# Kernel optimization log

Hardware: AMD Instinct MI355X
Metric: run time of the kernel (lower is better)

The kernel has to match this reference:

```python
import jax, jax.numpy as jnp
import numpy as np

B, T, H = 1, 2048, 2048
HEADS, DH = 16, 128  # head_dim = H // HEADS
K = 50               # block size
NEG = -1e9


def setup_inputs() -> dict:
    key = jax.random.key(0)
    ks = jax.random.split(key, 6)
    x = jax.random.normal(ks[0], (B, T, H), jnp.float32)
    mask = jnp.ones((B, T), jnp.float32)
    bias = jax.random.normal(ks[1], (B, HEADS, T, T), jnp.float32) * 0.02
    s = 1.0 / np.sqrt(H)
    Wq = jax.random.normal(ks[2], (H, HEADS, DH), jnp.float32) * s
    Wk = jax.random.normal(ks[3], (H, HEADS, DH), jnp.float32) * s
    Wv = jax.random.normal(ks[4], (H, HEADS, DH), jnp.float32) * s
    Wo = jax.random.normal(ks[5], (HEADS, DH, H), jnp.float32) * (1.0 / np.sqrt(H))
    return {"x_BxTxH": x, "mask_BxT": mask, "attention_bias_BxHxTxT": bias,
            "Wq": Wq, "Wk": Wk, "Wv": Wv, "Wo": Wo}


def _local_self_attention(x, mask, bias, Wq, Wk, Wv, Wo):
    b, t, h = x.shape
    extra = K - t % K          # module always pads (pads a full block if t % K == 0)
    p = t + extra
    n = p // K
    # pad + block the inputs: [b, n, K, h]
    xb = jnp.pad(x, ((0, 0), (0, extra), (0, 0))).reshape(b, n, K, h)
    # pad mask with -1e9 (as in the module), block, build pairwise mask via multiply
    mb = jnp.pad(mask, ((0, 0), (0, extra)), constant_values=NEG).reshape(b, n, K)
    pair = mb[..., :, None] * mb[..., None, :]              # [b, n, K, K]
    mask_bias = jnp.where(pair > 0, 0.0, NEG)[:, :, None]   # [b, n, 1, K, K] (broadcast heads)
    # pad attention bias and extract block-diagonal: [b, n, heads, K, K]
    bp = jnp.pad(bias, ((0, 0), (0, 0), (0, extra), (0, extra)))
    nb = bp.reshape(b, HEADS, n, K, n, K)
    idx = jnp.arange(n)
    blk_bias = nb[:, :, idx, :, idx, :]          # [n, b, heads, K, K]
    blk_bias = jnp.transpose(blk_bias, (1, 0, 2, 3, 4))  # [b, n, heads, K, K]
    # per-block multi-head attention (no qkv bias, query scaled by head_dim**-0.5)
    q = jnp.einsum('bnkh,hef->bnkef', xb, Wq) * (DH ** -0.5)
    k = jnp.einsum('bnkh,hef->bnkef', xb, Wk)
    v = jnp.einsum('bnkh,hef->bnkef', xb, Wv)
    logits = jnp.einsum('bnqef,bnkef->bneqk', q, k) + blk_bias + mask_bias
    attn = jax.nn.softmax(logits, axis=-1)
    out = jnp.einsum('bneqk,bnkef->bnqef', attn, v)
    out = jnp.einsum('bnqef,efh->bnqh', out, Wo).reshape(b, p, h)
    return out[:, :t, :]


def reference(x_BxTxH, mask_BxT, attention_bias_BxHxTxT, Wq, Wk, Wv, Wo):
    return _local_self_attention(x_BxTxH, mask_BxT, attention_bias_BxHxTxT, Wq, Wk, Wv, Wo)
```

## Files before the change

kernel.cpp:

```cpp
#include <hip/hip_runtime.h>
#include <hip/hip_bf16.h>

typedef _Float16 f16x8 __attribute__((ext_vector_type(8)));
typedef float f32x4 __attribute__((ext_vector_type(4)));

#define T_DIM 2048
#define H_DIM 2048
#define N_HEADS 16
#define DH 128
#define KBLK 50
#define NBLK 41
#define NEGV (-1.0e9f)
#define QSCALE 0.08838834764831845f

__device__ __forceinline__ void gl_lds16(const void* g, void* l) {
    __builtin_amdgcn_global_load_lds(
        (const __attribute__((address_space(1))) void*)g,
        (__attribute__((address_space(3))) void*)l, 16, 0, 0);
}

__global__ __launch_bounds__(256) void prep_kernel(const float* __restrict__ x,
                                                   const float* __restrict__ Wq,
                                                   const float* __restrict__ Wk,
                                                   const float* __restrict__ Wv,
                                                   const float* __restrict__ Wo,
                                                   _Float16* __restrict__ xb,
                                                   _Float16* __restrict__ WT,
                                                   _Float16* __restrict__ WoT) {
    __shared__ float tile[32][33];
    int z = blockIdx.z;
    int tx = threadIdx.x, ty = threadIdx.y;
    if (z == 4) {
        if (blockIdx.y >= 32) return;
        int flat = blockIdx.y * 64 + blockIdx.x;
        int i = (flat * 256 + ty * 32 + tx) * 8;
        float4 a = *(const float4*)&x[i];
        float4 b = *(const float4*)&x[i + 4];
        f16x8 o = {(_Float16)a.x, (_Float16)a.y, (_Float16)a.z, (_Float16)a.w,
                   (_Float16)b.x, (_Float16)b.y, (_Float16)b.z, (_Float16)b.w};
        *(f16x8*)&xb[i] = o;
        return;
    }
    const float* src = (z == 0) ? Wq : (z == 1) ? Wk : (z == 2) ? Wv : Wo;
    _Float16* dst = (z == 3) ? WoT : (WT + (size_t)z * T_DIM * H_DIM);
    int bx = blockIdx.x * 32, by = blockIdx.y * 32;
#pragma unroll
    for (int i = 0; i < 4; i++)
        tile[ty + i * 8][tx] = src[(size_t)(by + ty + i * 8) * H_DIM + bx + tx];
    __syncthreads();
#pragma unroll
    for (int i = 0; i < 4; i++)
        dst[(size_t)(bx + ty + i * 8) * H_DIM + by + tx] = (_Float16)tile[tx][ty + i * 8];
}

__global__ __launch_bounds__(512, 2) void qkv192_kernel(const _Float16* __restrict__ A,
                                                        const _Float16* __restrict__ BT,
                                                        _Float16* __restrict__ qkv) {
    const int K = 2048, NT = 32;
    __shared__ _Float16 smem[57344];
    _Float16* sA0 = smem;
    _Float16* sA1 = smem + 16384;
    _Float16* sB0 = smem + 32768;
    _Float16* sB1 = smem + 45056;

    int tid = threadIdx.x;
    int lane = tid & 63, wave = tid >> 6;
    int wm = wave >> 2, wn = wave & 3;
    int cb = lane & 15, hi = lane >> 4;

    int bid = blockIdx.x;
    int swz = (bid & 7) * 32 + (bid >> 3);
    int by = swz >> 5, bx = swz & 31;
    int bm = by * 256, bn = bx * 192;

    f32x4 acc[8][3];
#pragma unroll
    for (int m = 0; m < 8; m++)
#pragma unroll
        for (int n = 0; n < 3; n++) acc[m][n] = (f32x4){0.f, 0.f, 0.f, 0.f};

    int rp = tid >> 3, cc = tid & 7;
    int scol = ((cc ^ (rp & 7)) << 3);

    auto stageA = [&](int t, int u) {
        int buf = t & 1;
        gl_lds16(A + (size_t)(bm + u * 64 + rp) * K + (t << 6) + scol,
                 (buf ? sA1 : sA0) + u * 4096 + tid * 8);
    };
    auto stageB = [&](int t, int u) {
        int buf = t & 1;
        gl_lds16(BT + (size_t)(bn + u * 64 + rp) * K + (t << 6) + scol,
                 (buf ? sB1 : sB0) + u * 4096 + tid * 8);
    };

    f16x8 a_lo[4][2], a_hi[4][2], b01[2][2], b2[2];

    stageA(0, 0); stageA(0, 1); stageA(0, 2); stageA(0, 3);
    stageB(0, 0); stageB(0, 1); stageB(0, 2);
    stageA(1, 0); stageA(1, 1); stageA(1, 2); stageA(1, 3);
    asm volatile("s_waitcnt vmcnt(4)" ::: "memory");
    __builtin_amdgcn_s_barrier();

    for (int t = 0; t < NT; t++) {
        int buf = t & 1;
        const char* bA = (const char*)(buf ? sA1 : sA0);
        const char* bB = (const char*)(buf ? sB1 : sB0);
#pragma unroll
        for (int mf = 0; mf < 4; mf++) {
            int ra = wm * 128 + mf * 16 + cb;
#pragma unroll
            for (int ks = 0; ks < 2; ks++)
                a_lo[mf][ks] = *(const f16x8*)(bA + (ra << 7) +
                                               ((ks * 64 + hi * 16) ^ ((ra & 7) << 4)));
        }
#pragma unroll
        for (int nf = 0; nf < 2; nf++) {
            int rb = wn * 48 + nf * 16 + cb;
#pragma unroll
            for (int ks = 0; ks < 2; ks++)
                b01[nf][ks] = *(const f16x8*)(bB + (rb << 7) +
                                              ((ks * 64 + hi * 16) ^ ((rb & 7) << 4)));
        }
        if (t + 1 < NT) { stageB(t + 1, 0); stageB(t + 1, 1); }
        __builtin_amdgcn_s_barrier();
        asm volatile("s_waitcnt lgkmcnt(0)" ::: "memory");
        __builtin_amdgcn_s_setprio(1);
#pragma unroll
        for (int mf = 0; mf < 4; mf++)
#pragma unroll
            for (int nf = 0; nf < 2; nf++)
#pragma unroll
                for (int ks = 0; ks < 2; ks++)
                    acc[mf][nf] = __builtin_amdgcn_mfma_f32_16x16x32_f16(a_lo[mf][ks], b01[nf][ks], acc[mf][nf], 0, 0, 0);
        __builtin_amdgcn_s_setprio(0);
        __builtin_amdgcn_s_barrier();

#pragma unroll
        for (int mf = 0; mf < 4; mf++) {
            int ra = wm * 128 + 64 + mf * 16 + cb;
#pragma unroll
            for (int ks = 0; ks < 2; ks++)
                a_hi[mf][ks] = *(const f16x8*)(bA + (ra << 7) +
                                               ((ks * 64 + hi * 16) ^ ((ra & 7) << 4)));
        }
        {
            int rb = wn * 48 + 32 + cb;
#pragma unroll
            for (int ks = 0; ks < 2; ks++)
                b2[ks] = *(const f16x8*)(bB + (rb << 7) +
                                         ((ks * 64 + hi * 16) ^ ((rb & 7) << 4)));
        }
        if (t + 1 < NT) stageB(t + 1, 2);
        __builtin_amdgcn_s_barrier();
        asm volatile("s_waitcnt lgkmcnt(0)" ::: "memory");
        __builtin_amdgcn_s_setprio(1);
#pragma unroll
        for (int mf = 0; mf < 4; mf++)
#pragma unroll
            for (int ks = 0; ks < 2; ks++)
                acc[4 + mf][2] = __builtin_amdgcn_mfma_f32_16x16x32_f16(a_hi[mf][ks], b2[ks], acc[4 + mf][2], 0, 0, 0);
        __builtin_amdgcn_s_setprio(0);
        __builtin_amdgcn_s_barrier();

        if (t + 2 < NT) { stageA(t + 2, 0); stageA(t + 2, 1); }
        __builtin_amdgcn_s_barrier();
        __builtin_amdgcn_s_setprio(1);
#pragma unroll
        for (int mf = 0; mf < 4; mf++)
#pragma unroll
            for (int ks = 0; ks < 2; ks++)
                acc[mf][2] = __builtin_amdgcn_mfma_f32_16x16x32_f16(a_lo[mf][ks], b2[ks], acc[mf][2], 0, 0, 0);
        __builtin_amdgcn_s_setprio(0);
        __builtin_amdgcn_s_barrier();

        if (t + 2 < NT) { stageA(t + 2, 2); stageA(t + 2, 3); }
        if (t < NT - 2)
            asm volatile("s_waitcnt vmcnt(4)" ::: "memory");
        else if (t == NT - 2)
            asm volatile("s_waitcnt vmcnt(0)" ::: "memory");
        __builtin_amdgcn_s_barrier();
        __builtin_amdgcn_s_setprio(1);
#pragma unroll
        for (int mf = 0; mf < 4; mf++)
#pragma unroll
            for (int nf = 0; nf < 2; nf++)
#pragma unroll
                for (int ks = 0; ks < 2; ks++)
                    acc[4 + mf][nf] = __builtin_amdgcn_mfma_f32_16x16x32_f16(a_hi[mf][ks], b01[nf][ks], acc[4 + mf][nf], 0, 0, 0);
        __builtin_amdgcn_s_setprio(0);
        __builtin_amdgcn_s_barrier();
    }

#pragma unroll
    for (int p = 0; p < 2; p++) {
        if (p) __builtin_amdgcn_s_barrier();
        if (wm == p) {
#pragma unroll
            for (int mf = 0; mf < 8; mf++)
#pragma unroll
                for (int nf = 0; nf < 3; nf++) {
                    int col = wn * 48 + nf * 16 + cb;
                    float sc = ((bn + col) >> 11) == 0 ? QSCALE : 1.0f;
#pragma unroll
                    for (int r = 0; r < 4; r++) {
                        int row = mf * 16 + hi * 4 + r;
                        smem[row * 200 + col] = (_Float16)(acc[mf][nf][r] * sc);
                    }
                }
        }
        __builtin_amdgcn_s_barrier();
#pragma unroll
        for (int it = 0; it < 6; it++) {
            int c = it * 512 + tid;
            int row = c / 24, col8 = c - row * 24;
            int gm = bm + p * 128 + row;
            int gn = bn + col8 * 8;
            int tensor = gn >> 11;
            int ef = gn & 2047;
            int e = ef >> 7, f0 = ef & 127;
            uint4 v = *(const uint4*)&smem[row * 200 + col8 * 8];
            *(uint4*)(qkv + (size_t)tensor * (T_DIM * H_DIM) + (size_t)e * (T_DIM * DH) +
                      (size_t)gm * DH + f0) = v;
        }
    }
}

__global__ __launch_bounds__(512, 2) void oproj_kernel(const _Float16* __restrict__ A,
                                                       const _Float16* __restrict__ BT,
                                                       _Float16* __restrict__ part) {
    const int K = 2048, NT = 8;
    __shared__ _Float16 smem[65536];
    _Float16* sA0 = smem;
    _Float16* sA1 = smem + 16384;
    _Float16* sB0 = smem + 32768;
    _Float16* sB1 = smem + 49152;

    int tid = threadIdx.x;
    int lane = tid & 63, wave = tid >> 6;
    int wm = wave >> 2, wn = wave & 3;
    int cb = lane & 15, hi = lane >> 4;

    int bid = blockIdx.x;
    int s = bid & 3, tile = bid >> 2;
    int by = tile >> 3, bx = tile & 7;
    int bm = by * 256, bn = bx * 256;
    int kbase = s * 512;

    f32x4 acc[8][4];
#pragma unroll
    for (int m = 0; m < 8; m++)
#pragma unroll
        for (int n = 0; n < 4; n++) acc[m][n] = (f32x4){0.f, 0.f, 0.f, 0.f};

    auto stageP = [&](int t, int p) {
        int buf = t & 1, k0 = kbase + (t << 6);
        const _Float16* src = (p < 2) ? A + (size_t)(bm + ((p & 1) << 7)) * K + k0
                                      : BT + (size_t)(bn + ((p & 1) << 7)) * K + k0;
        _Float16* dst = ((p < 2) ? (buf ? sA1 : sA0) : (buf ? sB1 : sB0)) + ((p & 1) << 13);
#pragma unroll
        for (int l = 0; l < 2; l++) {
            int c = l * 512 + tid;
            int rp = c >> 3, cc = c & 7;
            int col = (cc ^ (rp & 7)) << 3;
            gl_lds16(src + (size_t)rp * K + col, dst + c * 8);
        }
    };

    f16x8 a_lo[4][2], a_hi[4][2], b_lo[2][2], b_hi[2][2];

    stageP(0, 0); stageP(0, 1); stageP(0, 2); stageP(0, 3);
    stageP(1, 0); stageP(1, 1);
    asm volatile("s_waitcnt vmcnt(4)" ::: "memory");
    __builtin_amdgcn_s_barrier();

    for (int t = 0; t < NT; t++) {
        int buf = t & 1;
        const char* bA = (const char*)(buf ? sA1 : sA0);
        const char* bB = (const char*)(buf ? sB1 : sB0);
#pragma unroll
        for (int m = 0; m < 4; m++) {
            int ra = wm * 128 + m * 16 + cb;
#pragma unroll
            for (int ks = 0; ks < 2; ks++)
                a_lo[m][ks] = *(const f16x8*)(bA + (ra << 7) +
                                              ((ks * 64 + hi * 16) ^ ((ra & 7) << 4)));
        }
#pragma unroll
        for (int n = 0; n < 2; n++) {
            int rb = wn * 64 + n * 16 + cb;
#pragma unroll
            for (int ks = 0; ks < 2; ks++)
                b_lo[n][ks] = *(const f16x8*)(bB + (rb << 7) +
                                              ((ks * 64 + hi * 16) ^ ((rb & 7) << 4)));
        }
        if (t + 1 < NT) stageP(t + 1, 2);
        __builtin_amdgcn_s_barrier();
        asm volatile("s_waitcnt lgkmcnt(0)" ::: "memory");
        __builtin_amdgcn_s_setprio(1);
#pragma unroll
        for (int m = 0; m < 4; m++)
#pragma unroll
            for (int n = 0; n < 2; n++)
#pragma unroll
                for (int ks = 0; ks < 2; ks++)
                    acc[m][n] = __builtin_amdgcn_mfma_f32_16x16x32_f16(a_lo[m][ks], b_lo[n][ks], acc[m][n], 0, 0, 0);
        __builtin_amdgcn_s_setprio(0);
        __builtin_amdgcn_s_barrier();

#pragma unroll
        for (int m = 0; m < 4; m++) {
            int ra = wm * 128 + 64 + m * 16 + cb;
#pragma unroll
            for (int ks = 0; ks < 2; ks++)
                a_hi[m][ks] = *(const f16x8*)(bA + (ra << 7) +
                                              ((ks * 64 + hi * 16) ^ ((ra & 7) << 4)));
        }
#pragma unroll
        for (int n = 0; n < 2; n++) {
            int rb = wn * 64 + 32 + n * 16 + cb;
#pragma unroll
            for (int ks = 0; ks < 2; ks++)
                b_hi[n][ks] = *(const f16x8*)(bB + (rb << 7) +
                                              ((ks * 64 + hi * 16) ^ ((rb & 7) << 4)));
        }
        if (t + 1 < NT) stageP(t + 1, 3);
        __builtin_amdgcn_s_barrier();
        asm volatile("s_waitcnt lgkmcnt(0)" ::: "memory");
        __builtin_amdgcn_s_setprio(1);
#pragma unroll
        for (int m = 0; m < 4; m++)
#pragma unroll
            for (int n = 0; n < 2; n++)
#pragma unroll
                for (int ks = 0; ks < 2; ks++)
                    acc[4 + m][2 + n] = __builtin_amdgcn_mfma_f32_16x16x32_f16(a_hi[m][ks], b_hi[n][ks], acc[4 + m][2 + n], 0, 0, 0);
        __builtin_amdgcn_s_setprio(0);
        __builtin_amdgcn_s_barrier();

        if (t + 2 < NT) stageP(t + 2, 0);
        __builtin_amdgcn_s_barrier();
        __builtin_amdgcn_s_setprio(1);
#pragma unroll
        for (int m = 0; m < 4; m++)
#pragma unroll
            for (int n = 0; n < 2; n++)
#pragma unroll
                for (int ks = 0; ks < 2; ks++)
                    acc[m][2 + n] = __builtin_amdgcn_mfma_f32_16x16x32_f16(a_lo[m][ks], b_hi[n][ks], acc[m][2 + n], 0, 0, 0);
        __builtin_amdgcn_s_setprio(0);
        __builtin_amdgcn_s_barrier();

        if (t + 2 < NT) stageP(t + 2, 1);
        if (t < NT - 2)
            asm volatile("s_waitcnt vmcnt(4)" ::: "memory");
        else if (t == NT - 2)
            asm volatile("s_waitcnt vmcnt(0)" ::: "memory");
        __builtin_amdgcn_s_barrier();
        __builtin_amdgcn_s_setprio(1);
#pragma unroll
        for (int m = 0; m < 4; m++)
#pragma unroll
            for (int n = 0; n < 2; n++)
#pragma unroll
                for (int ks = 0; ks < 2; ks++)
                    acc[4 + m][n] = __builtin_amdgcn_mfma_f32_16x16x32_f16(a_hi[m][ks], b_lo[n][ks], acc[4 + m][n], 0, 0, 0);
        __builtin_amdgcn_s_setprio(0);
        __builtin_amdgcn_s_barrier();
    }

    _Float16* pb = part + (size_t)s * T_DIM * H_DIM;
#pragma unroll
    for (int p = 0; p < 2; p++) {
        if (p) __builtin_amdgcn_s_barrier();
        if (wm == p) {
#pragma unroll
            for (int m = 0; m < 8; m++)
#pragma unroll
                for (int n = 0; n < 4; n++) {
                    int col = wn * 64 + ((n & 1) * 16) + ((n >> 1) * 32) + cb;
#pragma unroll
                    for (int r = 0; r < 4; r++) {
                        int row = ((m & 3) * 16) + ((m >> 2) * 64) + hi * 4 + r;
                        smem[row * 264 + col] = (_Float16)acc[m][n][r];
                    }
                }
        }
        __builtin_amdgcn_s_barrier();
#pragma unroll
        for (int it = 0; it < 8; it++) {
            int c = it * 512 + tid;
            int row = c >> 5, col8 = c & 31;
            int gm = bm + p * 128 + row;
            int gn = bn + col8 * 8;
            uint4 v = *(const uint4*)&smem[row * 264 + col8 * 8];
            *(uint4*)&pb[(size_t)gm * H_DIM + gn] = v;
        }
    }
}

__global__ __launch_bounds__(256) void reduce4_kernel(const _Float16* __restrict__ part,
                                                      float* __restrict__ out) {
    const size_t S = (size_t)T_DIM * H_DIM;
    int i = (blockIdx.x * 256 + threadIdx.x) * 8;
    f16x8 p0 = *(const f16x8*)&part[i];
    f16x8 p1 = *(const f16x8*)&part[S + i];
    f16x8 p2 = *(const f16x8*)&part[2 * S + i];
    f16x8 p3 = *(const f16x8*)&part[3 * S + i];
#pragma unroll
    for (int j = 0; j < 8; j++)
        out[i + j] = (float)p0[j] + (float)p1[j] + (float)p2[j] + (float)p3[j];
}

__global__ __launch_bounds__(256) void attn_kernel(const _Float16* __restrict__ qkvb,
                                                   const float* __restrict__ bias,
                                                   const float* __restrict__ mask,
                                                   _Float16* __restrict__ aout) {
    int bid = blockIdx.x;
    int n = bid >> 4, e = bid & 15;
    int t0 = n * KBLK;
    int valid = (T_DIM - t0 < KBLK) ? (T_DIM - t0) : KBLK;

    __shared__ _Float16 Qs[64 * 136];
    __shared__ _Float16 Ks[64 * 136];
    __shared__ _Float16 VTs[128 * 72];
    __shared__ _Float16 Ps[64 * 72];
    __shared__ float maskv[64];

    int tid = threadIdx.x;
    int lane = tid & 63, wave = tid >> 6;
    const _Float16* qp = qkvb + (size_t)e * (T_DIM * DH);
    const _Float16* kp = qkvb + (size_t)(T_DIM * H_DIM) + (size_t)e * (T_DIM * DH);
    const _Float16* vp = qkvb + (size_t)2 * (T_DIM * H_DIM) + (size_t)e * (T_DIM * DH);

#pragma unroll
    for (int i = 0; i < 4; i++) {
        int c = tid + i * 256;
        int r = c >> 4, c8 = c & 15;
        uint4 z = {0u, 0u, 0u, 0u};
        uint4 vq = z, vk = z;
        if (r < valid) {
            vq = *(const uint4*)&qp[(size_t)(t0 + r) * DH + c8 * 8];
            vk = *(const uint4*)&kp[(size_t)(t0 + r) * DH + c8 * 8];
        }
        *(uint4*)&Qs[r * 136 + c8 * 8] = vq;
        *(uint4*)&Ks[r * 136 + c8 * 8] = vk;
    }
#pragma unroll
    for (int i = 0; i < 4; i++) {
        int c = tid + i * 256;
        int r = c & 63;
        int f0 = (c >> 6) * 8;
        uint4 v = {0u, 0u, 0u, 0u};
        if (r < valid) v = *(const uint4*)&vp[(size_t)(t0 + r) * DH + f0];
        _Float16 tmp[8];
        *(uint4*)tmp = v;
#pragma unroll
        for (int j = 0; j < 8; j++) VTs[(f0 + j) * 72 + r] = tmp[j];
    }
    if (tid < 64) maskv[tid] = (tid < valid) ? mask[t0 + tid] : NEGV;
    __syncthreads();

    int qr0 = wave * 16;
    int cb = lane & 15, hi = lane >> 4;

    f16x8 aq[4];
#pragma unroll
    for (int ks = 0; ks < 4; ks++)
        aq[ks] = *(const f16x8*)&Qs[(qr0 + cb) * 136 + ks * 32 + hi * 8];
    f32x4 s[4];
#pragma unroll
    for (int kt = 0; kt < 4; kt++) s[kt] = (f32x4){0.f, 0.f, 0.f, 0.f};
#pragma unroll
    for (int kt = 0; kt < 4; kt++)
#pragma unroll
        for (int ks = 0; ks < 4; ks++) {
            f16x8 bk = *(const f16x8*)&Ks[(kt * 16 + cb) * 136 + ks * 32 + hi * 8];
            s[kt] = __builtin_amdgcn_mfma_f32_16x16x32_f16(aq[ks], bk, s[kt], 0, 0, 0);
        }

#pragma unroll
    for (int r = 0; r < 4; r++) {
        int rl = qr0 + hi * 4 + r;
        int qi = t0 + rl;
        float mq = maskv[rl];
        float lg[4];
        float mx = -3.4e38f;
#pragma unroll
        for (int kt = 0; kt < 4; kt++) {
            int cl = kt * 16 + cb, ki = t0 + cl;
            float bg = (qi < T_DIM && ki < T_DIM)
                           ? bias[((size_t)e * T_DIM + qi) * T_DIM + ki] : 0.f;
            float pr = mq * maskv[cl];
            float v = s[kt][r] + bg + (pr > 0.f ? 0.f : NEGV);
            lg[kt] = v;
            mx = fmaxf(mx, v);
        }
#pragma unroll
        for (int off = 8; off; off >>= 1) mx = fmaxf(mx, __shfl_xor(mx, off));
        float sum = 0.f;
#pragma unroll
        for (int kt = 0; kt < 4; kt++) {
            float pe = __expf(lg[kt] - mx);
            lg[kt] = pe;
            sum += pe;
        }
#pragma unroll
        for (int off = 8; off; off >>= 1) sum += __shfl_xor(sum, off);
        float inv = 1.f / sum;
#pragma unroll
        for (int kt = 0; kt < 4; kt++)
            Ps[rl * 72 + kt * 16 + cb] = (_Float16)(lg[kt] * inv);
    }
    __syncthreads();

    f16x8 pa[2];
#pragma unroll
    for (int ks = 0; ks < 2; ks++)
        pa[ks] = *(const f16x8*)&Ps[(qr0 + cb) * 72 + ks * 32 + hi * 8];
#pragma unroll
    for (int ft = 0; ft < 8; ft++) {
        f32x4 o = (f32x4){0.f, 0.f, 0.f, 0.f};
#pragma unroll
        for (int ks = 0; ks < 2; ks++) {
            f16x8 bv = *(const f16x8*)&VTs[(ft * 16 + cb) * 72 + ks * 32 + hi * 8];
            o = __builtin_amdgcn_mfma_f32_16x16x32_f16(pa[ks], bv, o, 0, 0, 0);
        }
#pragma unroll
        for (int r = 0; r < 4; r++) {
            int rl = qr0 + hi * 4 + r;
            if (rl < valid)
                aout[(size_t)(t0 + rl) * H_DIM + e * DH + ft * 16 + cb] = (_Float16)o[r];
        }
    }
}

extern "C" void kernel_launch(void* const* d_in, const int* in_sizes, int n_in,
                              void* d_out, int out_size, void* d_ws, size_t ws_size,
                              hipStream_t stream) {
    const float* x    = (const float*)d_in[0];
    const float* mask = (const float*)d_in[1];
    const float* bias = (const float*)d_in[2];
    const float* Wq   = (const float*)d_in[3];
    const float* Wk   = (const float*)d_in[4];
    const float* Wv   = (const float*)d_in[5];
    const float* Wo   = (const float*)d_in[6];
    float* out = (float*)d_out;

    _Float16* xb   = (_Float16*)d_ws;
    _Float16* WT   = xb + (size_t)T_DIM * H_DIM;
    _Float16* WoT  = WT + (size_t)3 * T_DIM * H_DIM;
    _Float16* qkvb = WoT + (size_t)T_DIM * H_DIM;
    _Float16* aout = qkvb + (size_t)3 * T_DIM * H_DIM;
    _Float16* part = aout + (size_t)T_DIM * H_DIM;

    prep_kernel<<<dim3(64, 64, 5), dim3(32, 8), 0, stream>>>(x, Wq, Wk, Wv, Wo, xb, WT, WoT);

    qkv192_kernel<<<256, 512, 0, stream>>>(xb, WT, qkvb);

    attn_kernel<<<NBLK * N_HEADS, 256, 0, stream>>>(qkvb, bias, mask, aout);

    oproj_kernel<<<256, 512, 0, stream>>>(aout, WoT, part);
    reduce4_kernel<<<(T_DIM * H_DIM) / (256 * 8), 256, 0, stream>>>(part, out);
}
```

Baseline: 127.0 us.

## Replace split-K output projection with 128x128 full-K tiles writing fp32 directly

The output projection no longer splits K four ways into fp16 partial buffers followed by a separate reduce kernel. Each block now computes a 128x128 tile over the full K=2048, using a three-stage LDS ring with 64-wide K steps, and stores fp32 results straight to the output. This removes the partial-buffer writes and reads and one kernel launch. In exchange each tile has lower arithmetic intensity and the loop runs 32 iterations instead of 8. The epilogue also writes scalar, strided fp32 stores with no LDS staging.

```diff
diff --git a/kernel.cpp b/kernel.cpp
--- a/kernel.cpp
+++ b/kernel.cpp
@@ -225,15 +225,11 @@
     }
 }
 
-__global__ __launch_bounds__(512, 2) void oproj_kernel(const _Float16* __restrict__ A,
+__global__ __launch_bounds__(512, 1) void oproj_kernel(const _Float16* __restrict__ A,
                                                        const _Float16* __restrict__ BT,
-                                                       _Float16* __restrict__ part) {
-    const int K = 2048, NT = 8;
-    __shared__ _Float16 smem[65536];
-    _Float16* sA0 = smem;
-    _Float16* sA1 = smem + 16384;
-    _Float16* sB0 = smem + 32768;
-    _Float16* sB1 = smem + 49152;
+                                                       float* __restrict__ out) {
+    const int K = 2048, NT = 32;
+    __shared__ _Float16 smem[49152];
 
     int tid = threadIdx.x;
     int lane = tid & 63, wave = tid >> 6;
@@ -241,174 +237,100 @@
     int cb = lane & 15, hi = lane >> 4;
 
     int bid = blockIdx.x;
-    int s = bid & 3, tile = bid >> 2;
-    int by = tile >> 3, bx = tile & 7;
-    int bm = by * 256, bn = bx * 256;
-    int kbase = s * 512;
-
-    f32x4 acc[8][4];
-#pragma unroll
-    for (int m = 0; m < 8; m++)
-#pragma unroll
-        for (int n = 0; n < 4; n++) acc[m][n] = (f32x4){0.f, 0.f, 0.f, 0.f};
-
-    auto stageP = [&](int t, int p) {
-        int buf = t & 1, k0 = kbase + (t << 6);
-        const _Float16* src = (p < 2) ? A + (size_t)(bm + ((p & 1) << 7)) * K + k0
-                                      : BT + (size_t)(bn + ((p & 1) << 7)) * K + k0;
-        _Float16* dst = ((p < 2) ? (buf ? sA1 : sA0) : (buf ? sB1 : sB0)) + ((p & 1) << 13);
-#pragma unroll
-        for (int l = 0; l < 2; l++) {
-            int c = l * 512 + tid;
-            int rp = c >> 3, cc = c & 7;
-            int col = (cc ^ (rp & 7)) << 3;
-            gl_lds16(src + (size_t)rp * K + col, dst + c * 8);
-        }
+    int by = bid >> 4, bx = bid & 15;
+    int bm = by * 128, bn = bx * 128;
+
+    f32x4 acc[4][2];
+#pragma unroll
+    for (int m = 0; m < 4; m++)
+#pragma unroll
+        for (int n = 0; n < 2; n++) acc[m][n] = (f32x4){0.f, 0.f, 0.f, 0.f};
+
+    int rp = tid >> 3, cc = tid & 7;
+    int scol = ((cc ^ (rp & 7)) << 3);
+
+    auto bufp = [&](int t) { return smem + (t % 3) * 16384; };
+    auto stageA = [&](int t, int u) {
+        gl_lds16(A + (size_t)(bm + u * 64 + rp) * K + (t << 6) + scol,
+                 bufp(t) + u * 4096 + tid * 8);
     };
-
-    f16x8 a_lo[4][2], a_hi[4][2], b_lo[2][2], b_hi[2][2];
-
-    stageP(0, 0); stageP(0, 1); stageP(0, 2); stageP(0, 3);
-    stageP(1, 0); stageP(1, 1);
+    auto stageB = [&](int t, int u) {
+        gl_lds16(BT + (size_t)(bn + u * 64 + rp) * K + (t << 6) + scol,
+                 bufp(t) + 8192 + u * 4096 + tid * 8);
+    };
+
+    f16x8 a[4][2], b0[2], b1[2];
+
+    stageA(0, 0); stageA(0, 1); stageB(0, 0); stageB(0, 1);
+    stageA(1, 0); stageA(1, 1); stageB(1, 0); stageB(1, 1);
     asm volatile("s_waitcnt vmcnt(4)" ::: "memory");
     __builtin_amdgcn_s_barrier();
 
     for (int t = 0; t < NT; t++) {
-        int buf = t & 1;
-        const char* bA = (const char*)(buf ? sA1 : sA0);
-        const char* bB = (const char*)(buf ? sB1 : sB0);
-#pragma unroll
-        for (int m = 0; m < 4; m++) {
-            int ra = wm * 128 + m * 16 + cb;
-#pragma unroll
-            for (int ks = 0; ks < 2; ks++)
-                a_lo[m][ks] = *(const f16x8*)(bA + (ra << 7) +
-                                              ((ks * 64 + hi * 16) ^ ((ra & 7) << 4)));
-        }
-#pragma unroll
-        for (int n = 0; n < 2; n++) {
-            int rb = wn * 64 + n * 16 + cb;
-#pragma unroll
-            for (int ks = 0; ks < 2; ks++)
-                b_lo[n][ks] = *(const f16x8*)(bB + (rb << 7) +
-                                              ((ks * 64 + hi * 16) ^ ((rb & 7) << 4)));
-        }
-        if (t + 1 < NT) stageP(t + 1, 2);
+        const char* bA = (const char*)bufp(t);
+        const char* bB = bA + 16384;
+#pragma unroll
+        for (int mf = 0; mf < 4; mf++) {
+            int ra = wm * 64 + mf * 16 + cb;
+#pragma unroll
+            for (int ks = 0; ks < 2; ks++)
+                a[mf][ks] = *(const f16x8*)(bA + (ra << 7) +
+                                            ((ks * 64 + hi * 16) ^ ((ra & 7) << 4)));
+        }
+        {
+            int rb = wn * 32 + cb;
+#pragma unroll
+            for (int ks = 0; ks < 2; ks++)
+                b0[ks] = *(const f16x8*)(bB + (rb << 7) +
+                                         ((ks * 64 + hi * 16) ^ ((rb & 7) << 4)));
+        }
+        if (t + 2 < NT) { stageA(t + 2, 0); stageA(t + 2, 1); }
         __builtin_amdgcn_s_barrier();
         asm volatile("s_waitcnt lgkmcnt(0)" ::: "memory");
         __builtin_amdgcn_s_setprio(1);
 #pragma unroll
-        for (int m = 0; m < 4; m++)
-#pragma unroll
-            for (int n = 0; n < 2; n++)
-#pragma unroll
-                for (int ks = 0; ks < 2; ks++)
-                    acc[m][n] = __builtin_amdgcn_mfma_f32_16x16x32_f16(a_lo[m][ks], b_lo[n][ks], acc[m][n], 0, 0, 0);
-        __builtin_amdgcn_s_setprio(0);
-        __builtin_amdgcn_s_barrier();
-
-#pragma unroll
-        for (int m = 0; m < 4; m++) {
-            int ra = wm * 128 + 64 + m * 16 + cb;
-#pragma unroll
-            for (int ks = 0; ks < 2; ks++)
-                a_hi[m][ks] = *(const f16x8*)(bA + (ra << 7) +
-                                              ((ks * 64 + hi * 16) ^ ((ra & 7) << 4)));
-        }
-#pragma unroll
-        for (int n = 0; n < 2; n++) {
-            int rb = wn * 64 + 32 + n * 16 + cb;
-#pragma unroll
-            for (int ks = 0; ks < 2; ks++)
-                b_hi[n][ks] = *(const f16x8*)(bB + (rb << 7) +
-                                              ((ks * 64 + hi * 16) ^ ((rb & 7) << 4)));
-        }
-        if (t + 1 < NT) stageP(t + 1, 3);
-        __builtin_amdgcn_s_barrier();
-        asm volatile("s_waitcnt lgkmcnt(0)" ::: "memory");
-        __builtin_amdgcn_s_setprio(1);
-#pragma unroll
-        for (int m = 0; m < 4; m++)
-#pragma unroll
-            for (int n = 0; n < 2; n++)
-#pragma unroll
-                for (int ks = 0; ks < 2; ks++)
-                    acc[4 + m][2 + n] = __builtin_amdgcn_mfma_f32_16x16x32_f16(a_hi[m][ks], b_hi[n][ks], acc[4 + m][2 + n], 0, 0, 0);
-        __builtin_amdgcn_s_setprio(0);
-        __builtin_amdgcn_s_barrier();
-
-        if (t + 2 < NT) stageP(t + 2, 0);
-        __builtin_amdgcn_s_barrier();
-        __builtin_amdgcn_s_setprio(1);
-#pragma unroll
-        for (int m = 0; m < 4; m++)
-#pragma unroll
-            for (int n = 0; n < 2; n++)
-#pragma unroll
-                for (int ks = 0; ks < 2; ks++)
-                    acc[m][2 + n] = __builtin_amdgcn_mfma_f32_16x16x32_f16(a_lo[m][ks], b_hi[n][ks], acc[m][2 + n], 0, 0, 0);
-        __builtin_amdgcn_s_setprio(0);
-        __builtin_amdgcn_s_barrier();
-
-        if (t + 2 < NT) stageP(t + 2, 1);
+        for (int mf = 0; mf < 4; mf++)
+#pragma unroll
+            for (int ks = 0; ks < 2; ks++)
+                acc[mf][0] = __builtin_amdgcn_mfma_f32_16x16x32_f16(a[mf][ks], b0[ks], acc[mf][0], 0, 0, 0);
+        __builtin_amdgcn_s_setprio(0);
+        __builtin_amdgcn_s_barrier();
+
+        {
+            int rb = wn * 32 + 16 + cb;
+#pragma unroll
+            for (int ks = 0; ks < 2; ks++)
+                b1[ks] = *(const f16x8*)(bB + (rb << 7) +
+                                         ((ks * 64 + hi * 16) ^ ((rb & 7) << 4)));
+        }
+        if (t + 2 < NT) { stageB(t + 2, 0); stageB(t + 2, 1); }
         if (t < NT - 2)
             asm volatile("s_waitcnt vmcnt(4)" ::: "memory");
         else if (t == NT - 2)
             asm volatile("s_waitcnt vmcnt(0)" ::: "memory");
         __builtin_amdgcn_s_barrier();
-        __builtin_amdgcn_s_setprio(1);
-#pragma unroll
-        for (int m = 0; m < 4; m++)
-#pragma unroll
-            for (int n = 0; n < 2; n++)
-#pragma unroll
-                for (int ks = 0; ks < 2; ks++)
-                    acc[4 + m][n] = __builtin_amdgcn_mfma_f32_16x16x32_f16(a_hi[m][ks], b_lo[n][ks], acc[4 + m][n], 0, 0, 0);
-        __builtin_amdgcn_s_setprio(0);
-        __builtin_amdgcn_s_barrier();
-    }
-
-    _Float16* pb = part + (size_t)s * T_DIM * H_DIM;
-#pragma unroll
-    for (int p = 0; p < 2; p++) {
-        if (p) __builtin_amdgcn_s_barrier();
-        if (wm == p) {
-#pragma unroll
-            for (int m = 0; m < 8; m++)
-#pragma unroll
-                for (int n = 0; n < 4; n++) {
-                    int col = wn * 64 + ((n & 1) * 16) + ((n >> 1) * 32) + cb;
-#pragma unroll
-                    for (int r = 0; r < 4; r++) {
-                        int row = ((m & 3) * 16) + ((m >> 2) * 64) + hi * 4 + r;
-                        smem[row * 264 + col] = (_Float16)acc[m][n][r];
-                    }
-                }
-        }
-        __builtin_amdgcn_s_barrier();
-#pragma unroll
-        for (int it = 0; it < 8; it++) {
-            int c = it * 512 + tid;
-            int row = c >> 5, col8 = c & 31;
-            int gm = bm + p * 128 + row;
-            int gn = bn + col8 * 8;
-            uint4 v = *(const uint4*)&smem[row * 264 + col8 * 8];
-            *(uint4*)&pb[(size_t)gm * H_DIM + gn] = v;
-        }
-    }
-}
-
-__global__ __launch_bounds__(256) void reduce4_kernel(const _Float16* __restrict__ part,
-                                                      float* __restrict__ out) {
-    const size_t S = (size_t)T_DIM * H_DIM;
-    int i = (blockIdx.x * 256 + threadIdx.x) * 8;
-    f16x8 p0 = *(const f16x8*)&part[i];
-    f16x8 p1 = *(const f16x8*)&part[S + i];
-    f16x8 p2 = *(const f16x8*)&part[2 * S + i];
-    f16x8 p3 = *(const f16x8*)&part[3 * S + i];
-#pragma unroll
-    for (int j = 0; j < 8; j++)
-        out[i + j] = (float)p0[j] + (float)p1[j] + (float)p2[j] + (float)p3[j];
+        asm volatile("s_waitcnt lgkmcnt(0)" ::: "memory");
+        __builtin_amdgcn_s_setprio(1);
+#pragma unroll
+        for (int mf = 0; mf < 4; mf++)
+#pragma unroll
+            for (int ks = 0; ks < 2; ks++)
+                acc[mf][1] = __builtin_amdgcn_mfma_f32_16x16x32_f16(a[mf][ks], b1[ks], acc[mf][1], 0, 0, 0);
+        __builtin_amdgcn_s_setprio(0);
+        __builtin_amdgcn_s_barrier();
+    }
+
+#pragma unroll
+    for (int mf = 0; mf < 4; mf++)
+#pragma unroll
+        for (int nf = 0; nf < 2; nf++) {
+            int gn = bn + wn * 32 + nf * 16 + cb;
+#pragma unroll
+            for (int r = 0; r < 4; r++) {
+                int gm = bm + wm * 64 + mf * 16 + hi * 4 + r;
+                out[(size_t)gm * H_DIM + gn] = acc[mf][nf][r];
+            }
+        }
 }
 
 __global__ __launch_bounds__(256) void attn_kernel(const _Float16* __restrict__ qkvb,
@@ -551,7 +473,6 @@
     _Float16* WoT  = WT + (size_t)3 * T_DIM * H_DIM;
     _Float16* qkvb = WoT + (size_t)T_DIM * H_DIM;
     _Float16* aout = qkvb + (size_t)3 * T_DIM * H_DIM;
-    _Float16* part = aout + (size_t)T_DIM * H_DIM;
 
     prep_kernel<<<dim3(64, 64, 5), dim3(32, 8), 0, stream>>>(x, Wq, Wk, Wv, Wo, xb, WT, WoT);
 
@@ -559,6 +480,5 @@
 
     attn_kernel<<<NBLK * N_HEADS, 256, 0, stream>>>(qkvb, bias, mask, aout);
 
-    oproj_kernel<<<256, 512, 0, stream>>>(aout, WoT, part);
-    reduce4_kernel<<<(T_DIM * H_DIM) / (256 * 8), 256, 0, stream>>>(part, out);
-}
+    oproj_kernel<<<256, 512, 0, stream>>>(aout, WoT, out);
+}
```

Measured after the change: 119.4 us. 6.0% less time.
